# Optimization experiments

Hardware: AMD Instinct MI355X
Metric: run time of the kernel (lower is better)

## Reference

```python
import jax, jax.numpy as jnp
import numpy as np
from jax import lax

N = 25600      # total nodes = G * T
E = 204800     # edges (before self loops)
IN_CH = 6
HID = 64
HEADS = 4
G = 512        # graphs per batch
T = 50         # sequence length (node_time in [0, T))
OUT = 30       # prediction_horizon * 3
NEG_SLOPE = 0.2
BN_EPS = 1e-5


def _gat(x, src, dst, W, a_src, a_dst, b, heads, outc):
    # PyG GATConv (concat=True): h = x W reshaped to (N, H, C)
    n = x.shape[0]
    h = (x @ W).reshape(n, heads, outc)
    # edge scores: leaky_relu(a_src . h_src + a_dst . h_dst), softmax over incoming edges of dst
    e = jax.nn.leaky_relu((h * a_src).sum(-1)[src] + (h * a_dst).sum(-1)[dst], NEG_SLOPE)  # (E, H)
    m = jax.ops.segment_max(e, dst, num_segments=n)
    ex = jnp.exp(e - m[dst])
    denom = jax.ops.segment_sum(ex, dst, num_segments=n)
    alpha = ex / denom[dst]
    out = jax.ops.segment_sum(alpha[:, :, None] * h[src], dst, num_segments=n)  # (N, H, C)
    return out.reshape(n, heads * outc) + b


def _bn_eval(x, g, b):
    # BatchNorm in eval with running_mean=0, running_var=1
    return g * (x * (1.0 / np.float32(np.sqrt(1.0 + BN_EPS)))) + b


def setup_inputs() -> dict:
    ks = jax.random.split(jax.random.key(0), 16)
    s = 0.1
    d = {}
    d["x"] = jax.random.normal(ks[0], (N, IN_CH), jnp.float32)
    d["edge_index"] = jax.random.randint(ks[1], (2, E), 0, N)
    idx = jnp.arange(N)
    d["batch"] = idx // T       # each graph has exactly T nodes
    d["node_time"] = idx % T
    d["W1"] = jax.random.normal(ks[2], (IN_CH, HEADS * HID), jnp.float32) * s
    d["att_src1"] = jax.random.normal(ks[3], (HEADS, HID), jnp.float32) * s
    d["att_dst1"] = jax.random.normal(ks[4], (HEADS, HID), jnp.float32) * s
    d["b1"] = jnp.zeros((HEADS * HID,), jnp.float32)
    d["g1"] = jnp.ones((HEADS * HID,), jnp.float32)
    d["be1"] = jnp.zeros((HEADS * HID,), jnp.float32)
    d["W2"] = jax.random.normal(ks[5], (HEADS * HID, HID), jnp.float32) * s
    d["att_src2"] = jax.random.normal(ks[6], (1, HID), jnp.float32) * s
    d["att_dst2"] = jax.random.normal(ks[7], (1, HID), jnp.float32) * s
    d["b2"] = jnp.zeros((HID,), jnp.float32)
    d["g2"] = jnp.ones((HID,), jnp.float32)
    d["be2"] = jnp.zeros((HID,), jnp.float32)
    d["Wih"] = jax.random.normal(ks[8], (4 * HID, HID), jnp.float32) * s
    d["Whh"] = jax.random.normal(ks[9], (4 * HID, HID), jnp.float32) * s
    d["bih"] = jnp.zeros((4 * HID,), jnp.float32)
    d["bhh"] = jnp.zeros((4 * HID,), jnp.float32)
    d["Wfc"] = jax.random.normal(ks[10], (HID, OUT), jnp.float32) * s
    d["bfc"] = jnp.zeros((OUT,), jnp.float32)
    return d


def reference(x, edge_index, batch, node_time, W1, att_src1, att_dst1, b1, g1, be1,
              W2, att_src2, att_dst2, b2, g2, be2, Wih, Whh, bih, bhh, Wfc, bfc):
    loops = jnp.arange(N)
    src = jnp.concatenate([edge_index[0], loops])  # GATConv adds self loops
    dst = jnp.concatenate([edge_index[1], loops])
    h = jax.nn.elu(_bn_eval(_gat(x, src, dst, W1, att_src1, att_dst1, b1, HEADS, HID), g1, be1))
    h = jax.nn.elu(_bn_eval(_gat(h, src, dst, W2, att_src2, att_dst2, b2, 1, HID), g2, be2))
    # vectorized replacement of the per-node python scatter loop
    x_seq = jnp.zeros((G, T, HID), h.dtype).at[batch, node_time].set(h)

    def step(carry, xt):
        hh, cc = carry
        gates = xt @ Wih.T + bih + hh @ Whh.T + bhh
        i, f, gg, o = jnp.split(gates, 4, axis=-1)
        cc = jax.nn.sigmoid(f) * cc + jax.nn.sigmoid(i) * jnp.tanh(gg)
        hh = jax.nn.sigmoid(o) * jnp.tanh(cc)
        return (hh, cc), None

    init = (jnp.zeros((G, HID), h.dtype), jnp.zeros((G, HID), h.dtype))
    (hn, _), _ = lax.scan(step, init, x_seq.transpose(1, 0, 2))  # scan over time
    return hn @ Wfc + bfc  # (G, 30)
```

## Files before the change

### kernel.cpp

```cpp
#include <hip/hip_runtime.h>

#define N_NODES 25600
#define N_EDGES 204800
#define EE (N_EDGES + N_NODES)
#define IN_CH 6
#define HID 64
#define HEADS 4
#define G_GRAPHS 512
#define T_STEPS 50
#define OUT_DIM 30
#define NEG_SLOPE 0.2f
#define BN_INV 0.9999950000374997f

__device__ __forceinline__ float lrelu_(float x){ return x > 0.f ? x : NEG_SLOPE * x; }
__device__ __forceinline__ float elu_(float x){ return x > 0.f ? x : __expf(x) - 1.f; }
__device__ __forceinline__ float sigmoid_(float x){
    return __builtin_amdgcn_rcpf(1.f + __expf(-x));
}
__device__ __forceinline__ float tanh_(float x){
    return 1.f - 2.f * __builtin_amdgcn_rcpf(1.f + __expf(2.f * x));
}

__global__ void count_k(const int* __restrict__ ei, int* __restrict__ counts){
    int e = blockIdx.x * 256 + threadIdx.x;
    if (e >= EE) return;
    int dst = (e < N_EDGES) ? ei[N_EDGES + e] : (e - N_EDGES);
    atomicAdd(&counts[dst], 1);
}

__global__ void scan_k(const int* __restrict__ counts, int* __restrict__ row_ptr,
                       int* __restrict__ cursor){
    __shared__ int part[1024];
    int t = threadIdx.x;
    const int CH = N_NODES / 1024;
    int base = t * CH;
    int s = 0;
    for (int i = 0; i < CH; i++) s += counts[base + i];
    part[t] = s;
    __syncthreads();
    for (int off = 1; off < 1024; off <<= 1){
        int v = (t >= off) ? part[t - off] : 0;
        __syncthreads();
        part[t] += v;
        __syncthreads();
    }
    int run = (t > 0) ? part[t - 1] : 0;
    for (int i = 0; i < CH; i++){
        int cv = counts[base + i];
        row_ptr[base + i] = run;
        cursor[base + i]  = run;
        run += cv;
    }
    if (t == 1023) row_ptr[N_NODES] = run;
}

__global__ void scatter_k(const int* __restrict__ ei, int* __restrict__ cursor,
                          int* __restrict__ ssrc){
    int e = blockIdx.x * 256 + threadIdx.x;
    if (e >= EE) return;
    int src, dst;
    if (e < N_EDGES){ src = ei[e]; dst = ei[N_EDGES + e]; }
    else            { src = dst = e - N_EDGES; }
    int pos = atomicAdd(&cursor[dst], 1);
    ssrc[pos] = src;
}

__global__ void ns_k(const float* __restrict__ x, const float* __restrict__ W1,
                     const float* __restrict__ asw, const float* __restrict__ adw,
                     float* __restrict__ as1, float* __restrict__ ad1){
    __shared__ float waS[IN_CH * 4], waD[IN_CH * 4];
    int t = threadIdx.x;
    if (t < 48){
        int k = t >> 3, h = (t >> 1) & 3, which = t & 1;
        const float* a = which ? adw : asw;
        float s = 0.f;
        #pragma unroll
        for (int c = 0; c < 64; c++) s += W1[k * 256 + h * 64 + c] * a[h * 64 + c];
        (which ? waD : waS)[k * 4 + h] = s;
    }
    __syncthreads();
    int n = blockIdx.x * 256 + t;
    float xv[IN_CH];
    #pragma unroll
    for (int k = 0; k < IN_CH; k++) xv[k] = x[n * IN_CH + k];
    float sv[4] = {0.f, 0.f, 0.f, 0.f}, dv[4] = {0.f, 0.f, 0.f, 0.f};
    #pragma unroll
    for (int k = 0; k < IN_CH; k++){
        #pragma unroll
        for (int h = 0; h < 4; h++){
            sv[h] += xv[k] * waS[k * 4 + h];
            dv[h] += xv[k] * waD[k * 4 + h];
        }
    }
    *(float4*)&as1[n * 4] = make_float4(sv[0], sv[1], sv[2], sv[3]);
    *(float4*)&ad1[n * 4] = make_float4(dv[0], dv[1], dv[2], dv[3]);
}

__global__ void gat1_aggx(const float* __restrict__ x, const float* __restrict__ as1,
                          const float* __restrict__ ad1, const int* __restrict__ row_ptr,
                          const int* __restrict__ ssrc, const float* __restrict__ W1,
                          const float* __restrict__ b1, const float* __restrict__ g1,
                          const float* __restrict__ be1, float* __restrict__ h1_act){
    __shared__ float w1s[IN_CH * 256];
    int tid = threadIdx.x;
    for (int i = tid; i < IN_CH * 256; i += 256) w1s[i] = W1[i];
    __syncthreads();
    int wv = tid >> 6, lane = tid & 63;
    int n = blockIdx.x * 4 + wv;
    int s0 = row_ptr[n], s1 = row_ptr[n + 1];
    float4 adn = *(const float4*)&ad1[n * 4];
    float xs0[IN_CH] = {}, xs1[IN_CH] = {}, xs2[IN_CH] = {}, xs3[IN_CH] = {};
    float d0 = 0.f, d1 = 0.f, d2 = 0.f, d3 = 0.f;
    int j = s0;
    for (; j + 2 <= s1; j += 2){
        int sa = ssrc[j], sb = ssrc[j + 1];
        float4 asa = *(const float4*)&as1[sa * 4];
        float4 asb = *(const float4*)&as1[sb * 4];
        const float2* xpa = (const float2*)(x + (size_t)sa * IN_CH);
        const float2* xpb = (const float2*)(x + (size_t)sb * IN_CH);
        float2 a0v = xpa[0], a1v = xpa[1], a2v = xpa[2];
        float2 b0v = xpb[0], b1v = xpb[1], b2v = xpb[2];
        float ea0 = __expf(lrelu_(asa.x + adn.x));
        float ea1 = __expf(lrelu_(asa.y + adn.y));
        float ea2 = __expf(lrelu_(asa.z + adn.z));
        float ea3 = __expf(lrelu_(asa.w + adn.w));
        float eb0 = __expf(lrelu_(asb.x + adn.x));
        float eb1 = __expf(lrelu_(asb.y + adn.y));
        float eb2 = __expf(lrelu_(asb.z + adn.z));
        float eb3 = __expf(lrelu_(asb.w + adn.w));
        d0 += ea0 + eb0; d1 += ea1 + eb1; d2 += ea2 + eb2; d3 += ea3 + eb3;
        float xa[IN_CH] = {a0v.x, a0v.y, a1v.x, a1v.y, a2v.x, a2v.y};
        float xb[IN_CH] = {b0v.x, b0v.y, b1v.x, b1v.y, b2v.x, b2v.y};
        #pragma unroll
        for (int k = 0; k < IN_CH; k++){
            xs0[k] += ea0 * xa[k] + eb0 * xb[k];
            xs1[k] += ea1 * xa[k] + eb1 * xb[k];
            xs2[k] += ea2 * xa[k] + eb2 * xb[k];
            xs3[k] += ea3 * xa[k] + eb3 * xb[k];
        }
    }
    for (; j < s1; j++){
        int s = ssrc[j];
        float4 as = *(const float4*)&as1[s * 4];
        float e0 = __expf(lrelu_(as.x + adn.x));
        float e1 = __expf(lrelu_(as.y + adn.y));
        float e2 = __expf(lrelu_(as.z + adn.z));
        float e3 = __expf(lrelu_(as.w + adn.w));
        d0 += e0; d1 += e1; d2 += e2; d3 += e3;
        const float2* xp = (const float2*)(x + (size_t)s * IN_CH);
        float2 xa = xp[0], xb = xp[1], xc = xp[2];
        float xv[IN_CH] = {xa.x, xa.y, xb.x, xb.y, xc.x, xc.y};
        #pragma unroll
        for (int k = 0; k < IN_CH; k++){
            xs0[k] += e0 * xv[k];
            xs1[k] += e1 * xv[k];
            xs2[k] += e2 * xv[k];
            xs3[k] += e3 * xv[k];
        }
    }
    float r0 = 1.f / d0, r1 = 1.f / d1, r2 = 1.f / d2, r3 = 1.f / d3;
    #pragma unroll
    for (int h = 0; h < 4; h++){
        const float* xsh = (h == 0) ? xs0 : (h == 1) ? xs1 : (h == 2) ? xs2 : xs3;
        float rh = (h == 0) ? r0 : (h == 1) ? r1 : (h == 2) ? r2 : r3;
        int col = h * 64 + lane;
        float acc = 0.f;
        #pragma unroll
        for (int k = 0; k < IN_CH; k++) acc += xsh[k] * w1s[k * 256 + col];
        float v = acc * rh + b1[col];
        v = g1[col] * (v * BN_INV) + be1[col];
        h1_act[(size_t)n * 256 + col] = elu_(v);
    }
}

#define TM 64
#define KT 32
#define APAD 4
__global__ __launch_bounds__(256) void gat2_tr(const float* __restrict__ h1_act,
                        const float* __restrict__ W2,
                        const float* __restrict__ asw, const float* __restrict__ adw,
                        float* __restrict__ h2_pre, float* __restrict__ as2,
                        float* __restrict__ ad2){
    __shared__ float As[TM][KT + APAD];
    __shared__ float Bs[KT][64];
    int tx = threadIdx.x;
    int rg = tx >> 4;
    int cg = tx & 15;
    int r0 = rg * 4, c0 = cg * 4;
    int rowBase = blockIdx.x * TM;
    float acc[4][4] = {};
    for (int k0 = 0; k0 < 256; k0 += KT){
        #pragma unroll
        for (int it = 0; it < 2; it++){
            int i = tx + it * 256;
            int row = i >> 3;
            int c4  = (i & 7) * 4;
            *(float4*)&As[row][c4] =
                *(const float4*)(h1_act + (size_t)(rowBase + row) * 256 + k0 + c4);
        }
        #pragma unroll
        for (int it = 0; it < 2; it++){
            int i = tx + it * 256;
            int row = i >> 4;
            int c4  = (i & 15) * 4;
            *(float4*)&Bs[row][c4] = *(const float4*)(W2 + (size_t)(k0 + row) * 64 + c4);
        }
        __syncthreads();
        #pragma unroll
        for (int kq = 0; kq < KT; kq += 4){
            float4 b0 = *(float4*)&Bs[kq + 0][c0];
            float4 b1v = *(float4*)&Bs[kq + 1][c0];
            float4 b2v = *(float4*)&Bs[kq + 2][c0];
            float4 b3 = *(float4*)&Bs[kq + 3][c0];
            #pragma unroll
            for (int i = 0; i < 4; i++){
                float4 a = *(float4*)&As[r0 + i][kq];
                acc[i][0] += a.x * b0.x + a.y * b1v.x + a.z * b2v.x + a.w * b3.x;
                acc[i][1] += a.x * b0.y + a.y * b1v.y + a.z * b2v.y + a.w * b3.y;
                acc[i][2] += a.x * b0.z + a.y * b1v.z + a.z * b2v.z + a.w * b3.z;
                acc[i][3] += a.x * b0.w + a.y * b1v.w + a.z * b2v.w + a.w * b3.w;
            }
        }
        __syncthreads();
    }
    float aw0 = asw[c0], aw1 = asw[c0+1], aw2 = asw[c0+2], aw3 = asw[c0+3];
    float dw0 = adw[c0], dw1 = adw[c0+1], dw2 = adw[c0+2], dw3 = adw[c0+3];
    #pragma unroll
    for (int i = 0; i < 4; i++){
        int row = rowBase + r0 + i;
        *(float4*)(h2_pre + (size_t)row * 64 + c0) =
            make_float4(acc[i][0], acc[i][1], acc[i][2], acc[i][3]);
        float sA = acc[i][0]*aw0 + acc[i][1]*aw1 + acc[i][2]*aw2 + acc[i][3]*aw3;
        float sD = acc[i][0]*dw0 + acc[i][1]*dw1 + acc[i][2]*dw2 + acc[i][3]*dw3;
        #pragma unroll
        for (int off = 8; off; off >>= 1){
            sA += __shfl_xor(sA, off);
            sD += __shfl_xor(sD, off);
        }
        if (cg == 0){ as2[row] = sA; ad2[row] = sD; }
    }
}

__global__ void gat2_agg(const float* __restrict__ h2_pre, const float* __restrict__ as2,
                         const float* __restrict__ ad2, const int* __restrict__ row_ptr,
                         const int* __restrict__ ssrc,
                         const float* __restrict__ b2, const float* __restrict__ g2,
                         const float* __restrict__ be2,
                         const int* __restrict__ batch, const int* __restrict__ ntime,
                         float* __restrict__ xseq){
    int wv = threadIdx.x >> 6, lane = threadIdx.x & 63;
    int n = blockIdx.x * 4 + wv;
    int s0 = row_ptr[n], s1 = row_ptr[n + 1];
    float adn = ad2[n];
    float denom = 0.f, acc = 0.f;
    int j = s0;
    for (; j + 4 <= s1; j += 4){
        int sa = ssrc[j], sb = ssrc[j + 1], sc = ssrc[j + 2], sd = ssrc[j + 3];
        float ea = __expf(lrelu_(as2[sa] + adn));
        float eb = __expf(lrelu_(as2[sb] + adn));
        float ec = __expf(lrelu_(as2[sc] + adn));
        float ed = __expf(lrelu_(as2[sd] + adn));
        float ha = h2_pre[(size_t)sa * 64 + lane];
        float hb = h2_pre[(size_t)sb * 64 + lane];
        float hc = h2_pre[(size_t)sc * 64 + lane];
        float hd = h2_pre[(size_t)sd * 64 + lane];
        denom += (ea + eb) + (ec + ed);
        acc += ea * ha + eb * hb + ec * hc + ed * hd;
    }
    for (; j < s1; j++){
        int s = ssrc[j];
        float e = __expf(lrelu_(as2[s] + adn));
        denom += e;
        acc += e * h2_pre[(size_t)s * 64 + lane];
    }
    float v = acc / denom + b2[lane];
    v = g2[lane] * (v * BN_INV) + be2[lane];
    v = elu_(v);
    int pos = batch[n] * T_STEPS + ntime[n];
    xseq[(size_t)pos * 64 + lane] = v;
}

__global__ __launch_bounds__(256) void gx_k(const float* __restrict__ xseq,
        const float* __restrict__ Wih, const float* __restrict__ bih,
        const float* __restrict__ bhh, float* __restrict__ gx){
    __shared__ float As[64][68];
    __shared__ float Bs[64][128];
    int tx = threadIdx.x;
    int rowBase = blockIdx.x * 64;
    int colBase = blockIdx.y * 128;
    #pragma unroll
    for (int it = 0; it < 4; it++){
        int i = tx + it * 256;
        int r = i >> 4;
        int c4 = (i & 15) * 4;
        *(float4*)&As[r][c4] = *(const float4*)(xseq + (size_t)(rowBase + r) * 64 + c4);
    }
    #pragma unroll
    for (int it = 0; it < 8; it++){
        int i = tx + it * 256;
        int jj = i & 127;
        int k4 = (i >> 7) * 4;
        float4 wv = *(const float4*)(Wih + (size_t)(colBase + jj) * 64 + k4);
        Bs[k4 + 0][jj] = wv.x;
        Bs[k4 + 1][jj] = wv.y;
        Bs[k4 + 2][jj] = wv.z;
        Bs[k4 + 3][jj] = wv.w;
    }
    __syncthreads();
    int rg = tx >> 5;
    int cg = tx & 31;
    int r0 = rg * 8, c0 = cg * 4;
    float acc[8][4] = {};
    #pragma unroll
    for (int kq = 0; kq < 64; kq += 4){
        float4 b0 = *(float4*)&Bs[kq + 0][c0];
        float4 b1 = *(float4*)&Bs[kq + 1][c0];
        float4 b2 = *(float4*)&Bs[kq + 2][c0];
        float4 b3 = *(float4*)&Bs[kq + 3][c0];
        #pragma unroll
        for (int i = 0; i < 8; i++){
            float4 a = *(float4*)&As[r0 + i][kq];
            acc[i][0] += a.x * b0.x + a.y * b1.x + a.z * b2.x + a.w * b3.x;
            acc[i][1] += a.x * b0.y + a.y * b1.y + a.z * b2.y + a.w * b3.y;
            acc[i][2] += a.x * b0.z + a.y * b1.z + a.z * b2.z + a.w * b3.z;
            acc[i][3] += a.x * b0.w + a.y * b1.w + a.z * b2.w + a.w * b3.w;
        }
    }
    int col = colBase + c0;
    float4 bb = make_float4(bih[col] + bhh[col], bih[col+1] + bhh[col+1],
                            bih[col+2] + bhh[col+2], bih[col+3] + bhh[col+3]);
    #pragma unroll
    for (int i = 0; i < 8; i++){
        int row = rowBase + r0 + i;
        *(float4*)(gx + (size_t)row * 256 + col) =
            make_float4(acc[i][0] + bb.x, acc[i][1] + bb.y,
                        acc[i][2] + bb.z, acc[i][3] + bb.w);
    }
}

__global__ __launch_bounds__(256, 2) void lstm_k(const float* __restrict__ gx,
        const float* __restrict__ Whh,
        const float* __restrict__ Wfc, const float* __restrict__ bfc,
        float* __restrict__ out){
    int g = blockIdx.x;
    int j = threadIdx.x;
    int wv = j >> 6, lane = j & 63;
    __shared__ float gates[2][256];
    __shared__ float hb[4][2][64];
    float4 whh[16];
    const float4* Hr = (const float4*)(Whh + j * 64);
    #pragma unroll
    for (int k = 0; k < 16; k++) whh[k] = Hr[k];
    float c = 0.f;
    hb[wv][0][lane] = 0.f;
    const float* gxg = gx + (size_t)g * T_STEPS * 256;
    float gxv = gxg[j];
    float hn = 0.f;
    for (int t = 0; t < T_STEPS; t++){
        float gx_next = (t + 1 < T_STEPS) ? gxg[(t + 1) * 256 + j] : 0.f;
        int buf = t & 1;
        const float4* hp = (const float4*)hb[wv][buf];
        float a0 = gxv, a1 = 0.f, a2 = 0.f, a3 = 0.f;
        #pragma unroll
        for (int k = 0; k < 16; k++){
            float4 hv = hp[k];
            float4 wvv = whh[k];
            a0 += wvv.x * hv.x;
            a1 += wvv.y * hv.y;
            a2 += wvv.z * hv.z;
            a3 += wvv.w * hv.w;
        }
        gates[buf][j] = (a0 + a1) + (a2 + a3);
        __syncthreads();
        float iv = gates[buf][lane];
        float fv = gates[buf][64 + lane];
        float gv = gates[buf][128 + lane];
        float ov = gates[buf][192 + lane];
        c = sigmoid_(fv) * c + sigmoid_(iv) * tanh_(gv);
        hn = sigmoid_(ov) * tanh_(c);
        hb[wv][buf ^ 1][lane] = hn;
        gxv = gx_next;
    }
    if (wv == 0) gates[0][lane] = hn;
    __syncthreads();
    if (j < OUT_DIM){
        float acc = bfc[j];
        #pragma unroll
        for (int k = 0; k < 64; k++) acc += gates[0][k] * Wfc[k * OUT_DIM + j];
        out[g * OUT_DIM + j] = acc;
    }
}

extern "C" void kernel_launch(void* const* d_in, const int* in_sizes, int n_in,
                              void* d_out, int out_size, void* d_ws, size_t ws_size,
                              hipStream_t stream){
    const float* x    = (const float*)d_in[0];
    const int*   ei   = (const int*)  d_in[1];
    const int*   batch= (const int*)  d_in[2];
    const int*   ntime= (const int*)  d_in[3];
    const float* W1   = (const float*)d_in[4];
    const float* as1w = (const float*)d_in[5];
    const float* ad1w = (const float*)d_in[6];
    const float* b1   = (const float*)d_in[7];
    const float* g1   = (const float*)d_in[8];
    const float* be1  = (const float*)d_in[9];
    const float* W2   = (const float*)d_in[10];
    const float* as2w = (const float*)d_in[11];
    const float* ad2w = (const float*)d_in[12];
    const float* b2   = (const float*)d_in[13];
    const float* g2   = (const float*)d_in[14];
    const float* be2  = (const float*)d_in[15];
    const float* Wih  = (const float*)d_in[16];
    const float* Whh  = (const float*)d_in[17];
    const float* bih  = (const float*)d_in[18];
    const float* bhh  = (const float*)d_in[19];
    const float* Wfc  = (const float*)d_in[20];
    const float* bfc  = (const float*)d_in[21];
    float* out = (float*)d_out;

    char* w = (char*)d_ws;
    auto alloc = [&](size_t bytes)->char*{
        char* p = w;
        w += (bytes + 255) & ~size_t(255);
        return p;
    };
    float* h1_act = (float*)alloc((size_t)N_NODES * 256 * 4);
    float* gx     = (float*)alloc((size_t)N_NODES * 256 * 4);
    float* h2_pre = (float*)alloc((size_t)N_NODES * 64 * 4);
    float* xseq   = (float*)alloc((size_t)G_GRAPHS * T_STEPS * 64 * 4);
    float* as1    = (float*)alloc((size_t)N_NODES * 4 * 4);
    float* ad1    = (float*)alloc((size_t)N_NODES * 4 * 4);
    float* as2    = (float*)alloc((size_t)N_NODES * 4);
    float* ad2    = (float*)alloc((size_t)N_NODES * 4);
    int* counts   = (int*)alloc((size_t)N_NODES * 4);
    int* row_ptr  = (int*)alloc((size_t)(N_NODES + 1) * 4);
    int* cursor   = (int*)alloc((size_t)N_NODES * 4);
    int* ssrc     = (int*)alloc((size_t)EE * 4);

    hipMemsetAsync(counts, 0, (size_t)N_NODES * 4, stream);
    count_k  <<<(EE + 255) / 256, 256, 0, stream>>>(ei, counts);
    scan_k   <<<1, 1024, 0, stream>>>(counts, row_ptr, cursor);
    scatter_k<<<(EE + 255) / 256, 256, 0, stream>>>(ei, cursor, ssrc);
    ns_k     <<<N_NODES / 256, 256, 0, stream>>>(x, W1, as1w, ad1w, as1, ad1);
    gat1_aggx<<<N_NODES / 4, 256, 0, stream>>>(x, as1, ad1, row_ptr, ssrc, W1, b1, g1, be1, h1_act);
    gat2_tr  <<<N_NODES / TM, 256, 0, stream>>>(h1_act, W2, as2w, ad2w, h2_pre, as2, ad2);
    gat2_agg <<<N_NODES / 4, 256, 0, stream>>>(h2_pre, as2, ad2, row_ptr, ssrc, b2, g2, be2, batch, ntime, xseq);
    gx_k     <<<dim3(N_NODES / 64, 2), 256, 0, stream>>>(xseq, Wih, bih, bhh, gx);
    lstm_k   <<<G_GRAPHS, 256, 0, stream>>>(gx, Whh, Wfc, bfc, out);
}
```

Before: 294.3 us.

## Precompute per-edge attention exps and batch two graphs per LSTM block

Adds es1_k/es2_k kernels that compute exponentiated attention scores once per edge in CSR order, so the aggregation kernels no longer recompute exp redundantly across all lanes of a wave. The scatter kernel also stores destination indices for these kernels. The LSTM kernel now processes two graphs per block, keeps Whh in swizzled shared memory, and broadcasts hidden state with readlane instead of going through shared memory. This adds extra launches and edge-sized buffers, and halves the LSTM grid.

After: 312.8 us. 1.06x slower.

```diff
diff --git a/kernel.cpp b/kernel.cpp
--- a/kernel.cpp
+++ b/kernel.cpp
@@ -20,6 +20,9 @@
 __device__ __forceinline__ float tanh_(float x){
     return 1.f - 2.f * __builtin_amdgcn_rcpf(1.f + __expf(2.f * x));
 }
+__device__ __forceinline__ float bcast_(float v, int l){
+    return __int_as_float(__builtin_amdgcn_readlane(__float_as_int(v), l));
+}
 
 __global__ void count_k(const int* __restrict__ ei, int* __restrict__ counts){
     int e = blockIdx.x * 256 + threadIdx.x;
@@ -55,7 +58,7 @@
 }
 
 __global__ void scatter_k(const int* __restrict__ ei, int* __restrict__ cursor,
-                          int* __restrict__ ssrc){
+                          int* __restrict__ ssrc, int* __restrict__ sdst){
     int e = blockIdx.x * 256 + threadIdx.x;
     if (e >= EE) return;
     int src, dst;
@@ -63,6 +66,7 @@
     else            { src = dst = e - N_EDGES; }
     int pos = atomicAdd(&cursor[dst], 1);
     ssrc[pos] = src;
+    sdst[pos] = dst;
 }
 
 __global__ void ns_k(const float* __restrict__ x, const float* __restrict__ W1,
@@ -96,8 +100,32 @@
     *(float4*)&ad1[n * 4] = make_float4(dv[0], dv[1], dv[2], dv[3]);
 }
 
-__global__ void gat1_aggx(const float* __restrict__ x, const float* __restrict__ as1,
-                          const float* __restrict__ ad1, const int* __restrict__ row_ptr,
+__global__ void es1_k(const float* __restrict__ as1, const float* __restrict__ ad1,
+                      const int* __restrict__ ssrc, const int* __restrict__ sdst,
+                      float* __restrict__ e1){
+    int p = blockIdx.x * 256 + threadIdx.x;
+    if (p >= EE) return;
+    int s = ssrc[p], d = sdst[p];
+    float4 as = *(const float4*)&as1[s * 4];
+    float4 ad = *(const float4*)&ad1[d * 4];
+    float4 e;
+    e.x = __expf(lrelu_(as.x + ad.x));
+    e.y = __expf(lrelu_(as.y + ad.y));
+    e.z = __expf(lrelu_(as.z + ad.z));
+    e.w = __expf(lrelu_(as.w + ad.w));
+    *(float4*)&e1[(size_t)p * 4] = e;
+}
+
+__global__ void es2_k(const float* __restrict__ as2, const float* __restrict__ ad2,
+                      const int* __restrict__ ssrc, const int* __restrict__ sdst,
+                      float* __restrict__ e2){
+    int p = blockIdx.x * 256 + threadIdx.x;
+    if (p >= EE) return;
+    e2[p] = __expf(lrelu_(as2[ssrc[p]] + ad2[sdst[p]]));
+}
+
+__global__ void gat1_aggx(const float* __restrict__ x, const float* __restrict__ e1,
+                          const int* __restrict__ row_ptr,
                           const int* __restrict__ ssrc, const float* __restrict__ W1,
                           const float* __restrict__ b1, const float* __restrict__ g1,
                           const float* __restrict__ be1, float* __restrict__ h1_act){
@@ -108,54 +136,41 @@
     int wv = tid >> 6, lane = tid & 63;
     int n = blockIdx.x * 4 + wv;
     int s0 = row_ptr[n], s1 = row_ptr[n + 1];
-    float4 adn = *(const float4*)&ad1[n * 4];
     float xs0[IN_CH] = {}, xs1[IN_CH] = {}, xs2[IN_CH] = {}, xs3[IN_CH] = {};
     float d0 = 0.f, d1 = 0.f, d2 = 0.f, d3 = 0.f;
     int j = s0;
     for (; j + 2 <= s1; j += 2){
         int sa = ssrc[j], sb = ssrc[j + 1];
-        float4 asa = *(const float4*)&as1[sa * 4];
-        float4 asb = *(const float4*)&as1[sb * 4];
+        float4 ea = *(const float4*)&e1[(size_t)j * 4];
+        float4 eb = *(const float4*)&e1[(size_t)(j + 1) * 4];
         const float2* xpa = (const float2*)(x + (size_t)sa * IN_CH);
         const float2* xpb = (const float2*)(x + (size_t)sb * IN_CH);
         float2 a0v = xpa[0], a1v = xpa[1], a2v = xpa[2];
         float2 b0v = xpb[0], b1v = xpb[1], b2v = xpb[2];
-        float ea0 = __expf(lrelu_(asa.x + adn.x));
-        float ea1 = __expf(lrelu_(asa.y + adn.y));
-        float ea2 = __expf(lrelu_(asa.z + adn.z));
-        float ea3 = __expf(lrelu_(asa.w + adn.w));
-        float eb0 = __expf(lrelu_(asb.x + adn.x));
-        float eb1 = __expf(lrelu_(asb.y + adn.y));
-        float eb2 = __expf(lrelu_(asb.z + adn.z));
-        float eb3 = __expf(lrelu_(asb.w + adn.w));
-        d0 += ea0 + eb0; d1 += ea1 + eb1; d2 += ea2 + eb2; d3 += ea3 + eb3;
+        d0 += ea.x + eb.x; d1 += ea.y + eb.y; d2 += ea.z + eb.z; d3 += ea.w + eb.w;
         float xa[IN_CH] = {a0v.x, a0v.y, a1v.x, a1v.y, a2v.x, a2v.y};
         float xb[IN_CH] = {b0v.x, b0v.y, b1v.x, b1v.y, b2v.x, b2v.y};
         #pragma unroll
         for (int k = 0; k < IN_CH; k++){
-            xs0[k] += ea0 * xa[k] + eb0 * xb[k];
-            xs1[k] += ea1 * xa[k] + eb1 * xb[k];
-            xs2[k] += ea2 * xa[k] + eb2 * xb[k];
-            xs3[k] += ea3 * xa[k] + eb3 * xb[k];
+            xs0[k] += ea.x * xa[k] + eb.x * xb[k];
+            xs1[k] += ea.y * xa[k] + eb.y * xb[k];
+            xs2[k] += ea.z * xa[k] + eb.z * xb[k];
+            xs3[k] += ea.w * xa[k] + eb.w * xb[k];
         }
     }
     for (; j < s1; j++){
         int s = ssrc[j];
-        float4 as = *(const float4*)&as1[s * 4];
-        float e0 = __expf(lrelu_(as.x + adn.x));
-        float e1 = __expf(lrelu_(as.y + adn.y));
-        float e2 = __expf(lrelu_(as.z + adn.z));
-        float e3 = __expf(lrelu_(as.w + adn.w));
-        d0 += e0; d1 += e1; d2 += e2; d3 += e3;
+        float4 e = *(const float4*)&e1[(size_t)j * 4];
+        d0 += e.x; d1 += e.y; d2 += e.z; d3 += e.w;
         const float2* xp = (const float2*)(x + (size_t)s * IN_CH);
         float2 xa = xp[0], xb = xp[1], xc = xp[2];
         float xv[IN_CH] = {xa.x, xa.y, xb.x, xb.y, xc.x, xc.y};
         #pragma unroll
         for (int k = 0; k < IN_CH; k++){
-            xs0[k] += e0 * xv[k];
-            xs1[k] += e1 * xv[k];
-            xs2[k] += e2 * xv[k];
-            xs3[k] += e3 * xv[k];
+            xs0[k] += e.x * xv[k];
+            xs1[k] += e.y * xv[k];
+            xs2[k] += e.z * xv[k];
+            xs3[k] += e.w * xv[k];
         }
     }
     float r0 = 1.f / d0, r1 = 1.f / d1, r2 = 1.f / d2, r3 = 1.f / d3;
@@ -241,9 +256,8 @@
     }
 }
 
-__global__ void gat2_agg(const float* __restrict__ h2_pre, const float* __restrict__ as2,
-                         const float* __restrict__ ad2, const int* __restrict__ row_ptr,
-                         const int* __restrict__ ssrc,
+__global__ void gat2_agg(const float* __restrict__ h2_pre, const float* __restrict__ e2,
+                         const int* __restrict__ row_ptr, const int* __restrict__ ssrc,
                          const float* __restrict__ b2, const float* __restrict__ g2,
                          const float* __restrict__ be2,
                          const int* __restrict__ batch, const int* __restrict__ ntime,
@@ -251,15 +265,11 @@
     int wv = threadIdx.x >> 6, lane = threadIdx.x & 63;
     int n = blockIdx.x * 4 + wv;
     int s0 = row_ptr[n], s1 = row_ptr[n + 1];
-    float adn = ad2[n];
     float denom = 0.f, acc = 0.f;
     int j = s0;
     for (; j + 4 <= s1; j += 4){
         int sa = ssrc[j], sb = ssrc[j + 1], sc = ssrc[j + 2], sd = ssrc[j + 3];
-        float ea = __expf(lrelu_(as2[sa] + adn));
-        float eb = __expf(lrelu_(as2[sb] + adn));
-        float ec = __expf(lrelu_(as2[sc] + adn));
-        float ed = __expf(lrelu_(as2[sd] + adn));
+        float ea = e2[j], eb = e2[j + 1], ec = e2[j + 2], ed = e2[j + 3];
         float ha = h2_pre[(size_t)sa * 64 + lane];
         float hb = h2_pre[(size_t)sb * 64 + lane];
         float hc = h2_pre[(size_t)sc * 64 + lane];
@@ -269,7 +279,7 @@
     }
     for (; j < s1; j++){
         int s = ssrc[j];
-        float e = __expf(lrelu_(as2[s] + adn));
+        float e = e2[j];
         denom += e;
         acc += e * h2_pre[(size_t)s * 64 + lane];
     }
@@ -338,56 +348,75 @@
     }
 }
 
-__global__ __launch_bounds__(256, 2) void lstm_k(const float* __restrict__ gx,
+__global__ __launch_bounds__(256) void lstm_k(const float* __restrict__ gx,
         const float* __restrict__ Whh,
         const float* __restrict__ Wfc, const float* __restrict__ bfc,
         float* __restrict__ out){
-    int g = blockIdx.x;
-    int j = threadIdx.x;
-    int wv = j >> 6, lane = j & 63;
-    __shared__ float gates[2][256];
-    __shared__ float hb[4][2][64];
-    float4 whh[16];
-    const float4* Hr = (const float4*)(Whh + j * 64);
-    #pragma unroll
-    for (int k = 0; k < 16; k++) whh[k] = Hr[k];
-    float c = 0.f;
-    hb[wv][0][lane] = 0.f;
-    const float* gxg = gx + (size_t)g * T_STEPS * 256;
-    float gxv = gxg[j];
-    float hn = 0.f;
+    __shared__ float wsh[256 * 64];
+    __shared__ float gates[2][2][256];
+    int g0 = blockIdx.x * 2;
+    int tx = threadIdx.x;
+    int lane = tx & 63, wv = tx >> 6;
+    {
+        const float4* src4 = (const float4*)(Whh + (size_t)tx * 64);
+        float4* dst4 = (float4*)(wsh + tx * 64);
+        #pragma unroll
+        for (int g = 0; g < 16; g++) dst4[g ^ (tx & 7)] = src4[g];
+    }
+    __syncthreads();
+    const float* gxA = gx + (size_t)g0 * T_STEPS * 256;
+    const float* gxB = gxA + (size_t)T_STEPS * 256;
+    const float4* w4 = (const float4*)(wsh + tx * 64);
+    int sw = tx & 7;
+    float cA = 0.f, hA = 0.f, cB = 0.f, hB = 0.f;
     for (int t = 0; t < T_STEPS; t++){
-        float gx_next = (t + 1 < T_STEPS) ? gxg[(t + 1) * 256 + j] : 0.f;
+        float ga = gxA[t * 256 + tx];
+        float gb = gxB[t * 256 + tx];
+        float a0 = ga, a1 = 0.f, a2 = 0.f, a3 = 0.f;
+        float b0 = gb, b1 = 0.f, b2 = 0.f, b3 = 0.f;
+        #pragma unroll
+        for (int gg = 0; gg < 16; gg++){
+            float4 w = w4[gg ^ sw];
+            int k = gg * 4;
+            a0 += w.x * bcast_(hA, k + 0);
+            a1 += w.y * bcast_(hA, k + 1);
+            a2 += w.z * bcast_(hA, k + 2);
+            a3 += w.w * bcast_(hA, k + 3);
+            b0 += w.x * bcast_(hB, k + 0);
+            b1 += w.y * bcast_(hB, k + 1);
+            b2 += w.z * bcast_(hB, k + 2);
+            b3 += w.w * bcast_(hB, k + 3);
+        }
         int buf = t & 1;
-        const float4* hp = (const float4*)hb[wv][buf];
-        float a0 = gxv, a1 = 0.f, a2 = 0.f, a3 = 0.f;
-        #pragma unroll
-        for (int k = 0; k < 16; k++){
-            float4 hv = hp[k];
-            float4 wvv = whh[k];
-            a0 += wvv.x * hv.x;
-            a1 += wvv.y * hv.y;
-            a2 += wvv.z * hv.z;
-            a3 += wvv.w * hv.w;
-        }
-        gates[buf][j] = (a0 + a1) + (a2 + a3);
+        gates[0][buf][tx] = (a0 + a1) + (a2 + a3);
+        gates[1][buf][tx] = (b0 + b1) + (b2 + b3);
         __syncthreads();
-        float iv = gates[buf][lane];
-        float fv = gates[buf][64 + lane];
-        float gv = gates[buf][128 + lane];
-        float ov = gates[buf][192 + lane];
-        c = sigmoid_(fv) * c + sigmoid_(iv) * tanh_(gv);
-        hn = sigmoid_(ov) * tanh_(c);
-        hb[wv][buf ^ 1][lane] = hn;
-        gxv = gx_next;
-    }
-    if (wv == 0) gates[0][lane] = hn;
-    __syncthreads();
-    if (j < OUT_DIM){
+        float iA = gates[0][buf][lane];
+        float fA = gates[0][buf][64 + lane];
+        float gA = gates[0][buf][128 + lane];
+        float oA = gates[0][buf][192 + lane];
+        float iB = gates[1][buf][lane];
+        float fB = gates[1][buf][64 + lane];
+        float gB = gates[1][buf][128 + lane];
+        float oB = gates[1][buf][192 + lane];
+        cA = sigmoid_(fA) * cA + sigmoid_(iA) * tanh_(gA);
+        hA = sigmoid_(oA) * tanh_(cA);
+        cB = sigmoid_(fB) * cB + sigmoid_(iB) * tanh_(gB);
+        hB = sigmoid_(oB) * tanh_(cB);
+    }
+    if (wv == 0){ gates[0][0][lane] = hA; gates[1][0][lane] = hB; }
+    __syncthreads();
+    if (tx < OUT_DIM){
+        float acc = bfc[tx];
+        #pragma unroll
+        for (int k = 0; k < 64; k++) acc += gates[0][0][k] * Wfc[k * OUT_DIM + tx];
+        out[g0 * OUT_DIM + tx] = acc;
+    } else if (tx >= 128 && tx < 128 + OUT_DIM){
+        int j = tx - 128;
         float acc = bfc[j];
         #pragma unroll
-        for (int k = 0; k < 64; k++) acc += gates[0][k] * Wfc[k * OUT_DIM + j];
-        out[g * OUT_DIM + j] = acc;
+        for (int k = 0; k < 64; k++) acc += gates[1][0][k] * Wfc[k * OUT_DIM + j];
+        out[(g0 + 1) * OUT_DIM + j] = acc;
     }
 }
 
@@ -428,6 +457,8 @@
     float* gx     = (float*)alloc((size_t)N_NODES * 256 * 4);
     float* h2_pre = (float*)alloc((size_t)N_NODES * 64 * 4);
     float* xseq   = (float*)alloc((size_t)G_GRAPHS * T_STEPS * 64 * 4);
+    float* e1     = (float*)alloc((size_t)EE * 4 * 4);
+    float* e2     = (float*)alloc((size_t)EE * 4);
     float* as1    = (float*)alloc((size_t)N_NODES * 4 * 4);
     float* ad1    = (float*)alloc((size_t)N_NODES * 4 * 4);
     float* as2    = (float*)alloc((size_t)N_NODES * 4);
@@ -436,15 +467,18 @@
     int* row_ptr  = (int*)alloc((size_t)(N_NODES + 1) * 4);
     int* cursor   = (int*)alloc((size_t)N_NODES * 4);
     int* ssrc     = (int*)alloc((size_t)EE * 4);
+    int* sdst     = (int*)alloc((size_t)EE * 4);
 
     hipMemsetAsync(counts, 0, (size_t)N_NODES * 4, stream);
     count_k  <<<(EE + 255) / 256, 256, 0, stream>>>(ei, counts);
     scan_k   <<<1, 1024, 0, stream>>>(counts, row_ptr, cursor);
-    scatter_k<<<(EE + 255) / 256, 256, 0, stream>>>(ei, cursor, ssrc);
+    scatter_k<<<(EE + 255) / 256, 256, 0, stream>>>(ei, cursor, ssrc, sdst);
     ns_k     <<<N_NODES / 256, 256, 0, stream>>>(x, W1, as1w, ad1w, as1, ad1);
-    gat1_aggx<<<N_NODES / 4, 256, 0, stream>>>(x, as1, ad1, row_ptr, ssrc, W1, b1, g1, be1, h1_act);
+    es1_k    <<<(EE + 255) / 256, 256, 0, stream>>>(as1, ad1, ssrc, sdst, e1);
+    gat1_aggx<<<N_NODES / 4, 256, 0, stream>>>(x, e1, row_ptr, ssrc, W1, b1, g1, be1, h1_act);
     gat2_tr  <<<N_NODES / TM, 256, 0, stream>>>(h1_act, W2, as2w, ad2w, h2_pre, as2, ad2);
-    gat2_agg <<<N_NODES / 4, 256, 0, stream>>>(h2_pre, as2, ad2, row_ptr, ssrc, b2, g2, be2, batch, ntime, xseq);
+    es2_k    <<<(EE + 255) / 256, 256, 0, stream>>>(as2, ad2, ssrc, sdst, e2);
+    gat2_agg <<<N_NODES / 4, 256, 0, stream>>>(h2_pre, e2, row_ptr, ssrc, b2, g2, be2, batch, ntime, xseq);
     gx_k     <<<dim3(N_NODES / 64, 2), 256, 0, stream>>>(xseq, Wih, bih, bhh, gx);
-    lstm_k   <<<G_GRAPHS, 256, 0, stream>>>(gx, Whh, Wfc, bfc, out);
-}
+    lstm_k   <<<G_GRAPHS / 2, 256, 0, stream>>>(gx, Whh, Wfc, bfc, out);
+}
```
